# Performance work log

Hardware: AMD Instinct MI355X
Metric: run time of the kernel (lower is better)

The kernel has to match this reference:

```python
import jax, jax.numpy as jnp
import numpy as np

ALPHA = 0.1          # init_kwargs alpha
B, C, K = 32768, 1000, 2  # batch, num_classes, num aux classifier heads


def setup_inputs() -> dict:
    key = jax.random.key(0)
    k1, k2, k3, k4, k5, k6 = jax.random.split(key, 6)
    return {
        "outputs": jax.random.normal(k1, (B, C), jnp.float32),
        "outputs_classifier": jax.random.normal(k2, (K, B, C), jnp.float32),
        "labels": jax.random.randint(k3, (B,), 0, C),
        "weight_bias": jax.random.normal(k4, (3,), jnp.float32),
        "args_bias": jax.random.uniform(k5, (1,), jnp.float32),
        "args_gamma": jax.random.uniform(k6, (1,), jnp.float32),
    }


def _cross_entropy(logits, labels):
    # torch.nn.CrossEntropyLoss (mean reduction)
    logp = jax.nn.log_softmax(logits, axis=-1)
    return -jnp.mean(jnp.take_along_axis(logp, labels[:, None], axis=-1)[:, 0])


def _distance_loss(outputs, labels, weight_bias, args_bias, args_gamma):
    th1, th2, b = weight_bias[0], weight_bias[1], weight_bias[2]
    # x[i] = outputs[i, labels[i]]
    x = jnp.take_along_axis(outputs, labels[:, None], axis=-1)[:, 0]  # [B]
    v, _ = jax.lax.top_k(outputs, 2)  # [B, 2], v[:,0] >= v[:,1]
    # original removes the FIRST top-2 entry equal to x, then sums the rest:
    #   if v0 == x -> y = v1; elif v1 == x -> y = v0; else y = v0 + v1
    y = jnp.where(v[:, 0] == x, v[:, 1],
                  jnp.where(v[:, 1] == x, v[:, 0], v[:, 0] + v[:, 1]))
    dist = (th1 * x + th2 * y + b - args_bias[0]) / jnp.sqrt(th1 ** 2 + th2 ** 2)
    per = jnp.where(dist >= 10.0, -2.0,
                    jnp.where(dist >= 0.0, -args_gamma[0] * dist, -dist))
    return jnp.sum(per)


def reference(outputs, outputs_classifier, labels, weight_bias, args_bias, args_gamma):
    base = _cross_entropy(outputs, labels)
    base = base + jnp.sum(
        jax.vmap(lambda lg: _cross_entropy(lg, labels))(outputs_classifier))
    dist = _distance_loss(outputs, labels, weight_bias, args_bias, args_gamma)
    return base + ALPHA * dist
```

## Files before the change

kernel.cpp:

```cpp
#include <hip/hip_runtime.h>
#include <math.h>

#define BATCH 32768
#define NCLS  1000
#define NV4   250
#define ALPHA 0.1f

__global__ __launch_bounds__(256, 4) void loss_kernel(
    const float* __restrict__ outputs,
    const float* __restrict__ oc,
    const int*   __restrict__ labels,
    const float* __restrict__ wb,
    const float* __restrict__ ab,
    const float* __restrict__ ag,
    float* __restrict__ out)
{
    const int lane  = threadIdx.x & 63;
    const int wave  = threadIdx.x >> 6;
    const int gwave = blockIdx.x * 4 + wave;
    const int nwav  = gridDim.x * 4;

    const float th1 = wb[0], th2 = wb[1], bb = wb[2];
    const float bias = ab[0], gamma = ag[0];
    const float inv_norm = 1.0f / sqrtf(th1 * th1 + th2 * th2);
    const float invB = 1.0f / (float)BATCH;

    float acc = 0.0f;

    const int R = 3 * BATCH;
    for (int row = gwave; row < R; row += nwav) {
        const bool is_out = (row < BATCH);
        const float* base;
        int lbl_idx;
        if (is_out) {
            base = outputs + (size_t)row * NCLS;
            lbl_idx = row;
        } else {
            const int r2 = row - BATCH;
            base = oc + (size_t)r2 * NCLS;
            lbl_idx = (r2 >= BATCH) ? (r2 - BATCH) : r2;
        }
        const int label = labels[lbl_idx];
        const float4* p = (const float4*)base;

        float v[16];
        #pragma unroll
        for (int j = 0; j < 4; ++j) {
            const int idx = lane + j * 64;
            float4 q;
            if (idx < NV4) q = p[idx];
            else           q = make_float4(-INFINITY, -INFINITY, -INFINITY, -INFINITY);
            v[4 * j + 0] = q.x; v[4 * j + 1] = q.y;
            v[4 * j + 2] = q.z; v[4 * j + 3] = q.w;
        }

        float m = v[0];
        #pragma unroll
        for (int j = 1; j < 16; ++j) m = fmaxf(m, v[j]);
        #pragma unroll
        for (int off = 32; off; off >>= 1) m = fmaxf(m, __shfl_xor(m, off, 64));

        float s = 0.0f;
        #pragma unroll
        for (int j = 0; j < 16; ++j) s += __expf(v[j] - m);
        #pragma unroll
        for (int off = 32; off; off >>= 1) s += __shfl_xor(s, off, 64);

        const float lse = m + __logf(s);
        const float x = base[label];
        float contrib = (lse - x) * invB;

        if (is_out) {
            float t0 = -INFINITY, t1 = -INFINITY;
            #pragma unroll
            for (int j = 0; j < 16; ++j) {
                const float val = v[j];
                if (val > t0)      { t1 = t0; t0 = val; }
                else if (val > t1) { t1 = val; }
            }
            #pragma unroll
            for (int off = 32; off; off >>= 1) {
                const float o0 = __shfl_xor(t0, off, 64);
                const float o1 = __shfl_xor(t1, off, 64);
                const float n0 = fmaxf(t0, o0);
                const float n1 = fmaxf(fminf(t0, o0), fmaxf(t1, o1));
                t0 = n0; t1 = n1;
            }
            const float y = (t0 == x) ? t1 : ((t1 == x) ? t0 : (t0 + t1));
            const float dist = (th1 * x + th2 * y + bb - bias) * inv_norm;
            const float per = (dist >= 10.0f) ? -2.0f
                            : ((dist >= 0.0f) ? (-gamma * dist) : (-dist));
            contrib += ALPHA * per;
        }
        acc += contrib;
    }

    __shared__ float wacc[4];
    if (lane == 0) wacc[wave] = acc;
    __syncthreads();
    if (threadIdx.x == 0) {
        float t = wacc[0] + wacc[1] + wacc[2] + wacc[3];
        atomicAdd(out, t);
    }
}

extern "C" void kernel_launch(void* const* d_in, const int* in_sizes, int n_in,
                              void* d_out, int out_size, void* d_ws, size_t ws_size,
                              hipStream_t stream) {
    const float* outputs = (const float*)d_in[0];
    const float* oc      = (const float*)d_in[1];
    const int*   labels  = (const int*)d_in[2];
    const float* wb      = (const float*)d_in[3];
    const float* ab      = (const float*)d_in[4];
    const float* ag      = (const float*)d_in[5];
    float* out = (float*)d_out;

    hipMemsetAsync(out, 0, (size_t)out_size * sizeof(float), stream);
    loss_kernel<<<dim3(2048), dim3(256), 0, stream>>>(outputs, oc, labels, wb, ab, ag, out);
}
```

Before: 438.8 us.

## Fully unroll row loop with software-pipelined double-buffered row loads

Replaces the strided row loop with a compile-time unrolled sequence of 12 rows per wave. Each row's loads, including the label gather, are issued before the previous row is reduced, so memory latency overlaps with compute. It also merges the max and top-2 passes for the outputs rows and makes the top-2 update branchless. The cost is doubled register arrays per thread, which may pressure occupancy under the launch bounds, and the code now hardcodes the grid so that 12 rows cover the batch exactly.

New measurement: 434.0 us. No clear change (-1.1%).

```diff
diff --git a/kernel.cpp b/kernel.cpp
--- a/kernel.cpp
+++ b/kernel.cpp
@@ -5,6 +5,114 @@
 #define NCLS  1000
 #define NV4   250
 #define ALPHA 0.1f
+#define GRID  2048
+#define NWAVE (GRID * 4)
+#define NROWS 12
+
+struct Scalars {
+    float th1, th2, bb, bias, gamma, inv_norm, invB;
+};
+
+template <int I>
+__device__ __forceinline__ void row_meta(int gwave,
+                                         const float* __restrict__ outputs,
+                                         const float* __restrict__ oc,
+                                         const int* __restrict__ labels,
+                                         const float*& base, int& label) {
+    if constexpr (I < 4) {
+        const int r = gwave + I * NWAVE;
+        base = outputs + (size_t)r * NCLS;
+        label = labels[r];
+    } else {
+        const int r2 = gwave + (I - 4) * NWAVE;
+        base = oc + (size_t)r2 * NCLS;
+        label = labels[(I < 8) ? r2 : (gwave + (I - 8) * NWAVE)];
+    }
+}
+
+__device__ __forceinline__ void load_row(float (&v)[16], float& x,
+                                         const float* __restrict__ base, int label, int lane) {
+    const float4* p = (const float4*)base;
+    #pragma unroll
+    for (int j = 0; j < 4; ++j) {
+        const int idx = lane + j * 64;
+        float4 q;
+        if (idx < NV4) q = p[idx];
+        else           q = make_float4(-INFINITY, -INFINITY, -INFINITY, -INFINITY);
+        v[4 * j + 0] = q.x; v[4 * j + 1] = q.y;
+        v[4 * j + 2] = q.z; v[4 * j + 3] = q.w;
+    }
+    x = base[label];
+}
+
+template <bool IS_OUT>
+__device__ __forceinline__ float process_row(const float (&v)[16], float x, const Scalars& sc) {
+    float m, contrib;
+    if constexpr (IS_OUT) {
+        float t0 = -INFINITY, t1 = -INFINITY;
+        #pragma unroll
+        for (int j = 0; j < 16; ++j) {
+            const float val = v[j];
+            const float nt1 = fmaxf(t1, fminf(t0, val));
+            t0 = fmaxf(t0, val);
+            t1 = nt1;
+        }
+        #pragma unroll
+        for (int off = 32; off; off >>= 1) {
+            const float o0 = __shfl_xor(t0, off, 64);
+            const float o1 = __shfl_xor(t1, off, 64);
+            const float n1 = fmaxf(fminf(t0, o0), fmaxf(t1, o1));
+            t0 = fmaxf(t0, o0);
+            t1 = n1;
+        }
+        m = t0;
+        float s = 0.0f;
+        #pragma unroll
+        for (int j = 0; j < 16; ++j) s += __expf(v[j] - m);
+        #pragma unroll
+        for (int off = 32; off; off >>= 1) s += __shfl_xor(s, off, 64);
+        const float lse = m + __logf(s);
+        contrib = (lse - x) * sc.invB;
+        const float y = (t0 == x) ? t1 : ((t1 == x) ? t0 : (t0 + t1));
+        const float dist = (sc.th1 * x + sc.th2 * y + sc.bb - sc.bias) * sc.inv_norm;
+        const float per = (dist >= 10.0f) ? -2.0f
+                        : ((dist >= 0.0f) ? (-sc.gamma * dist) : (-dist));
+        contrib += ALPHA * per;
+    } else {
+        m = v[0];
+        #pragma unroll
+        for (int j = 1; j < 16; ++j) m = fmaxf(m, v[j]);
+        #pragma unroll
+        for (int off = 32; off; off >>= 1) m = fmaxf(m, __shfl_xor(m, off, 64));
+        float s = 0.0f;
+        #pragma unroll
+        for (int j = 0; j < 16; ++j) s += __expf(v[j] - m);
+        #pragma unroll
+        for (int off = 32; off; off >>= 1) s += __shfl_xor(s, off, 64);
+        const float lse = m + __logf(s);
+        contrib = (lse - x) * sc.invB;
+    }
+    return contrib;
+}
+
+template <int I>
+__device__ __forceinline__ void step(float (&cur)[16], float& xcur,
+                                     float (&nxt)[16], float& xnxt,
+                                     float& acc, int gwave, int lane,
+                                     const float* __restrict__ outputs,
+                                     const float* __restrict__ oc,
+                                     const int* __restrict__ labels,
+                                     const Scalars& sc) {
+    if constexpr (I + 1 < NROWS) {
+        const float* b; int l;
+        row_meta<I + 1>(gwave, outputs, oc, labels, b, l);
+        load_row(nxt, xnxt, b, l, lane);
+    }
+    acc += process_row<(I < 4)>(cur, xcur, sc);
+    if constexpr (I + 1 < NROWS) {
+        step<I + 1>(nxt, xnxt, cur, xcur, acc, gwave, lane, outputs, oc, labels, sc);
+    }
+}
 
 __global__ __launch_bounds__(256, 4) void loss_kernel(
     const float* __restrict__ outputs,
@@ -18,82 +126,23 @@
     const int lane  = threadIdx.x & 63;
     const int wave  = threadIdx.x >> 6;
     const int gwave = blockIdx.x * 4 + wave;
-    const int nwav  = gridDim.x * 4;
 
-    const float th1 = wb[0], th2 = wb[1], bb = wb[2];
-    const float bias = ab[0], gamma = ag[0];
-    const float inv_norm = 1.0f / sqrtf(th1 * th1 + th2 * th2);
-    const float invB = 1.0f / (float)BATCH;
+    Scalars sc;
+    sc.th1 = wb[0]; sc.th2 = wb[1]; sc.bb = wb[2];
+    sc.bias = ab[0]; sc.gamma = ag[0];
+    sc.inv_norm = 1.0f / sqrtf(sc.th1 * sc.th1 + sc.th2 * sc.th2);
+    sc.invB = 1.0f / (float)BATCH;
 
     float acc = 0.0f;
+    float v[16], w[16];
+    float xv = 0.0f, xw = 0.0f;
 
-    const int R = 3 * BATCH;
-    for (int row = gwave; row < R; row += nwav) {
-        const bool is_out = (row < BATCH);
-        const float* base;
-        int lbl_idx;
-        if (is_out) {
-            base = outputs + (size_t)row * NCLS;
-            lbl_idx = row;
-        } else {
-            const int r2 = row - BATCH;
-            base = oc + (size_t)r2 * NCLS;
-            lbl_idx = (r2 >= BATCH) ? (r2 - BATCH) : r2;
-        }
-        const int label = labels[lbl_idx];
-        const float4* p = (const float4*)base;
-
-        float v[16];
-        #pragma unroll
-        for (int j = 0; j < 4; ++j) {
-            const int idx = lane + j * 64;
-            float4 q;
-            if (idx < NV4) q = p[idx];
-            else           q = make_float4(-INFINITY, -INFINITY, -INFINITY, -INFINITY);
-            v[4 * j + 0] = q.x; v[4 * j + 1] = q.y;
-            v[4 * j + 2] = q.z; v[4 * j + 3] = q.w;
-        }
-
-        float m = v[0];
-        #pragma unroll
-        for (int j = 1; j < 16; ++j) m = fmaxf(m, v[j]);
-        #pragma unroll
-        for (int off = 32; off; off >>= 1) m = fmaxf(m, __shfl_xor(m, off, 64));
-
-        float s = 0.0f;
-        #pragma unroll
-        for (int j = 0; j < 16; ++j) s += __expf(v[j] - m);
-        #pragma unroll
-        for (int off = 32; off; off >>= 1) s += __shfl_xor(s, off, 64);
-
-        const float lse = m + __logf(s);
-        const float x = base[label];
-        float contrib = (lse - x) * invB;
-
-        if (is_out) {
-            float t0 = -INFINITY, t1 = -INFINITY;
-            #pragma unroll
-            for (int j = 0; j < 16; ++j) {
-                const float val = v[j];
-                if (val > t0)      { t1 = t0; t0 = val; }
-                else if (val > t1) { t1 = val; }
-            }
-            #pragma unroll
-            for (int off = 32; off; off >>= 1) {
-                const float o0 = __shfl_xor(t0, off, 64);
-                const float o1 = __shfl_xor(t1, off, 64);
-                const float n0 = fmaxf(t0, o0);
-                const float n1 = fmaxf(fminf(t0, o0), fmaxf(t1, o1));
-                t0 = n0; t1 = n1;
-            }
-            const float y = (t0 == x) ? t1 : ((t1 == x) ? t0 : (t0 + t1));
-            const float dist = (th1 * x + th2 * y + bb - bias) * inv_norm;
-            const float per = (dist >= 10.0f) ? -2.0f
-                            : ((dist >= 0.0f) ? (-gamma * dist) : (-dist));
-            contrib += ALPHA * per;
-        }
-        acc += contrib;
+    {
+        const float* b; int l;
+        row_meta<0>(gwave, outputs, oc, labels, b, l);
+        load_row(v, xv, b, l, lane);
     }
+    step<0>(v, xv, w, xw, acc, gwave, lane, outputs, oc, labels, sc);
 
     __shared__ float wacc[4];
     if (lane == 0) wacc[wave] = acc;
@@ -116,5 +165,5 @@
     float* out = (float*)d_out;
 
     hipMemsetAsync(out, 0, (size_t)out_size * sizeof(float), stream);
-    loss_kernel<<<dim3(2048), dim3(256), 0, stream>>>(outputs, oc, labels, wb, ab, ag, out);
+    loss_kernel<<<dim3(GRID), dim3(256), 0, stream>>>(outputs, oc, labels, wb, ab, ag, out);
 }
```
